# Kernel optimization log

Hardware: AMD Instinct MI355X
Metric: run time of the kernel (lower is better)

The kernel has to match this reference:

```python
import jax, jax.numpy as jnp
import numpy as np

B, K, HH, WW = 512, 256, 16, 16   # batch, channels (K//2 of init K=512), latent H, W
KH = 128                          # GRU hidden size
F = 16                            # future_window_lin


def gru_forward(seq, h0, W_ih, W_hh, b_ih, b_hh):
    # seq: (B,T,K) batch_first, h0: (B,KH). PyTorch GRU gate order: r, z, n.
    gx = jnp.einsum('btk,gk->btg', seq, W_ih) + b_ih  # (B,T,3*KH)

    def step(h, gx_t):
        gh = h @ W_hh.T + b_hh
        xr, xz, xn = jnp.split(gx_t, 3, axis=-1)
        hr, hz, hn = jnp.split(gh, 3, axis=-1)
        r = jax.nn.sigmoid(xr + hr)
        z = jax.nn.sigmoid(xz + hz)
        n = jnp.tanh(xn + r * hn)
        h_new = (1.0 - z) * n + z * h
        return h_new, h_new

    hT, outs = jax.lax.scan(step, h0, jnp.swapaxes(gx, 0, 1))  # outs: (T,B,KH)
    return jnp.swapaxes(outs, 0, 1), hT


def setup_inputs() -> dict:
    key = jax.random.key(0)
    ks = jax.random.split(key, 9)
    s = 0.05
    return {
        'z_q_x_st': jax.random.normal(ks[0], (B, K, HH, WW), jnp.float32),
        'z_e_x': jax.random.normal(ks[1], (B, K, HH, WW), jnp.float32),
        'z_q_x': jax.random.normal(ks[2], (B, K, HH, WW), jnp.float32),
        'hidden': jnp.zeros((1, B, KH), jnp.float32),
        'W_ih': jax.random.normal(ks[3], (3 * KH, K), jnp.float32) * s,
        'W_hh': jax.random.normal(ks[4], (3 * KH, KH), jnp.float32) * s,
        'b_ih': jnp.zeros((3 * KH,), jnp.float32),
        'b_hh': jnp.zeros((3 * KH,), jnp.float32),
        'Wk_w': jax.random.normal(ks[5], (F, K, KH), jnp.float32) * s,
        'Wk_b': jnp.zeros((F, K), jnp.float32),
        'p_sample': 100,
    }


def reference(z_q_x_st, z_e_x, z_q_x, hidden, W_ih, W_hh, b_ih, b_hh, Wk_w, Wk_b, p_sample):
    batch, k, h, w = z_e_x.shape
    f = Wk_w.shape[0]
    # (B,K,H,W) -> (B,H*W,K); row = idx//W, col = idx%W is just the row-major flat index
    z_flat = jnp.transpose(z_q_x_st, (0, 2, 3, 1)).reshape(batch, h * w, k)
    # encoded samples at flat positions p_sample+1 .. p_sample+F  -> (F,B,K)
    encoded = jnp.swapaxes(z_flat[:, p_sample + 1: p_sample + 1 + f, :], 0, 1)
    # GRU over the causal prefix; c_t = output at step p_sample (the last one)
    seq = z_flat[:, : p_sample + 1, :]
    out, _ = gru_forward(seq, hidden[0], W_ih, W_hh, b_ih, b_hh)
    c_t = out[:, -1, :]  # (B,KH)
    # per-step linear heads, batched: (F,B,K)
    pred = jnp.einsum('fkh,bh->fbk', Wk_w, c_t) + Wk_b[:, None, :]
    # totals[i] = encoded[i] @ pred[i].T  -> (F,B,B)
    totals = jnp.einsum('fbk,fck->fbc', encoded, pred)
    lsm = jax.nn.log_softmax(totals, axis=2)
    diag_sum = jnp.sum(jnp.diagonal(lsm, axis1=1, axis2=2))
    nce = -diag_sum / (batch * f)
    # 'correct' only reflects the last loop iteration in the torch code
    last = totals[-1]
    sm = jax.nn.softmax(last, axis=1)       # softmax over dim=1, then argmax over dim=0
    preds_idx = jnp.argmax(sm, axis=0)
    correct = jnp.sum(preds_idx == jnp.arange(batch))
    accuracy = correct.astype(jnp.float32) / batch
    return accuracy, nce, z_e_x, z_q_x
```

## Files before the change

kernel.cpp:

```cpp
#include <hip/hip_runtime.h>
#include <math.h>

#define NB_B   512
#define NK     256
#define NKH    128
#define NG3    384
#define NT     101
#define NF     16
#define NPASS  (512ull*256*256)

#define OFF_GX   0ull
#define N_GX     (512ull*101*384)
#define OFF_CT   (OFF_GX + N_GX)
#define OFF_ENC  (OFF_CT + 512ull*128)
#define OFF_PRED (OFF_ENC + 16ull*512*256)
#define OFF_TOT  (OFF_PRED + 16ull*512*256)
#define OFF_LSE  (OFF_TOT + 16ull*512*512)
#define OFF_DML  (OFF_LSE + 8192ull)
#define OFF_WT   (OFF_DML + 8192ull)
#define OFF_WKT  (OFF_WT + 384ull*256)
#define OFF_CNT  (OFF_WKT + 16ull*128*256)

__global__ __launch_bounds__(256) void k_transpose(
    const float* __restrict__ W_ih, const float* __restrict__ Wk_w,
    float* __restrict__ Wt, float* __restrict__ Wkt, int* __restrict__ cnt) {
  int idx = blockIdx.x * 256 + threadIdx.x;
  if (idx == 0) *cnt = 0;
  if (idx < 384 * 256) {
    int g = idx % 384, k = idx / 384;
    Wt[idx] = W_ih[g * 256 + k];
  }
  if (idx < 16 * 128 * 256) {
    int k = idx & 255, h = (idx >> 8) & 127, f = idx >> 15;
    Wkt[idx] = Wk_w[(f * 256 + k) * 128 + h];
  }
}

__global__ __launch_bounds__(768) void k_gx(
    const float* __restrict__ zq, const float* __restrict__ Wt,
    const float* __restrict__ b_ih, float* __restrict__ gx) {
  __shared__ float Xs[64][104];
  int b = blockIdx.x;
  int tid = threadIdx.x;
  int g = tid % 384;
  int th = tid / 384;
  int lane = tid & 63, wid = tid >> 6;
  float acc[52];
#pragma unroll
  for (int i = 0; i < 52; i++) acc[i] = 0.f;
  const float* zb = zq + (size_t)b * 65536;
  for (int kc = 0; kc < 4; kc++) {
    __syncthreads();
    for (int k = wid; k < 64; k += 12) {
      int kk = kc * 64 + k;
      Xs[k][lane] = zb[kk * 256 + lane];
      int t1 = 64 + lane;
      if (t1 < 104) Xs[k][t1] = (t1 < 101) ? zb[kk * 256 + t1] : 0.f;
    }
    __syncthreads();
    for (int k = 0; k < 64; k++) {
      float w = Wt[(kc * 64 + k) * 384 + g];
      const float4* xp = (const float4*)&Xs[k][th * 52];
#pragma unroll
      for (int i = 0; i < 13; i++) {
        float4 x = xp[i];
        acc[4 * i + 0] += w * x.x;
        acc[4 * i + 1] += w * x.y;
        acc[4 * i + 2] += w * x.z;
        acc[4 * i + 3] += w * x.w;
      }
    }
  }
  float bias = b_ih[g];
  int t0 = th * 52;
#pragma unroll
  for (int i = 0; i < 52; i++) {
    int t = t0 + i;
    if (t < 101) gx[(size_t)t * (512 * 384) + b * 384 + g] = acc[i] + bias;
  }
}

__global__ __launch_bounds__(768) void k_scan(
    const float* __restrict__ gx, const float* __restrict__ W_hh,
    const float* __restrict__ b_hh, const float* __restrict__ hidden,
    float* __restrict__ ct,
    const float* __restrict__ src0, const float* __restrict__ src1,
    float2* __restrict__ d0, float2* __restrict__ d1) {
  int tid = threadIdx.x;
  if (blockIdx.x >= 256) {
    const float4* S0 = (const float4*)src0;
    const float4* S1 = (const float4*)src1;
    const size_t n4 = NPASS / 4;
    const size_t stride = 256ull * 768;
    for (size_t i = (size_t)(blockIdx.x - 256) * 768 + tid; i < n4; i += stride) {
      float4 a = S0[i];
      float4 b = S1[i];
      d0[2 * i]     = make_float2(a.x, a.y);
      d0[2 * i + 1] = make_float2(a.z, a.w);
      d1[2 * i]     = make_float2(b.x, b.y);
      d1[2 * i + 1] = make_float2(b.z, b.w);
    }
    return;
  }
  __shared__ float hs[2][128];
  __shared__ float ghp[2][2][384];
  int b0 = blockIdx.x * 2;
  int g = tid % 384, kh = tid / 384;
  float4 w[16];
  const float4* wp = (const float4*)(W_hh + g * 128 + kh * 64);
#pragma unroll
  for (int i = 0; i < 16; i++) w[i] = wp[i];
  if (tid < 256) {
    int r = tid >> 7, k = tid & 127;
    hs[r][k] = hidden[(b0 + r) * 128 + k];
  }
  __syncthreads();
  for (int t = 0; t < 101; t++) {
    const float4* h0 = (const float4*)&hs[0][kh * 64];
    const float4* h1 = (const float4*)&hs[1][kh * 64];
    float a0 = 0.f, a1 = 0.f;
#pragma unroll
    for (int i = 0; i < 16; i++) {
      float4 wv = w[i], x0 = h0[i], x1 = h1[i];
      a0 += wv.x * x0.x + wv.y * x0.y + wv.z * x0.z + wv.w * x0.w;
      a1 += wv.x * x1.x + wv.y * x1.y + wv.z * x1.z + wv.w * x1.w;
    }
    ghp[0][kh][g] = a0;
    ghp[1][kh][g] = a1;
    __syncthreads();
    if (tid < 256) {
      int r = tid >> 7, k = tid & 127;
      const float* gxb = gx + (size_t)t * (512 * 384) + (b0 + r) * 384;
      float xr = gxb[k], xz = gxb[128 + k], xn = gxb[256 + k];
      float hr = ghp[r][0][k] + ghp[r][1][k] + b_hh[k];
      float hz = ghp[r][0][128 + k] + ghp[r][1][128 + k] + b_hh[128 + k];
      float hn = ghp[r][0][256 + k] + ghp[r][1][256 + k] + b_hh[256 + k];
      float rr = 1.f / (1.f + __expf(-(xr + hr)));
      float zz = 1.f / (1.f + __expf(-(xz + hz)));
      float nn = tanhf(xn + rr * hn);
      hs[r][k] = (1.f - zz) * nn + zz * hs[r][k];
    }
    __syncthreads();
  }
  if (tid < 256) {
    int r = tid >> 7, k = tid & 127;
    ct[(b0 + r) * 128 + k] = hs[r][k];
  }
}

__global__ __launch_bounds__(256) void k_enc(const float* __restrict__ zq,
                                             float* __restrict__ enc) {
  __shared__ float tile[256][17];
  int b = blockIdx.x, tid = threadIdx.x;
  const float* zb = zq + (size_t)b * 65536;
  for (int pass = 0; pass < 16; pass++) {
    int idx = pass * 256 + tid;
    int k = idx >> 4, f = idx & 15;
    tile[k][f] = zb[k * 256 + 101 + f];
  }
  __syncthreads();
  for (int f = 0; f < 16; f++)
    enc[(size_t)f * 131072 + b * 256 + tid] = tile[tid][f];
}

__global__ __launch_bounds__(256) void k_pred(
    const float* __restrict__ Wkt, const float* __restrict__ Wk_b,
    const float* __restrict__ ct, float* __restrict__ pred) {
  __shared__ float cts[32][128];
  int f = blockIdx.x, c0 = blockIdx.y * 32;
  int tid = threadIdx.x;
  for (int pass = 0; pass < 16; pass++) {
    int idx = pass * 256 + tid;
    int cc = idx >> 7, h = idx & 127;
    cts[cc][h] = ct[(c0 + cc) * 128 + h];
  }
  __syncthreads();
  float acc[32];
#pragma unroll
  for (int i = 0; i < 32; i++) acc[i] = 0.f;
  const float* wb = Wkt + (size_t)f * 32768 + tid;
  for (int h = 0; h < 128; h += 4) {
    float w0 = wb[(h + 0) * 256], w1 = wb[(h + 1) * 256];
    float w2 = wb[(h + 2) * 256], w3 = wb[(h + 3) * 256];
#pragma unroll
    for (int cc = 0; cc < 32; cc++) {
      float4 cv = *(const float4*)&cts[cc][h];
      acc[cc] += w0 * cv.x + w1 * cv.y + w2 * cv.z + w3 * cv.w;
    }
  }
  float bias = Wk_b[f * 256 + tid];
#pragma unroll
  for (int cc = 0; cc < 32; cc++)
    pred[((size_t)f * 512 + c0 + cc) * 256 + tid] = acc[cc] + bias;
}

__global__ __launch_bounds__(256) void k_totals(
    const float* __restrict__ enc, const float* __restrict__ pred,
    float* __restrict__ tot) {
  __shared__ float As[32][68];
  __shared__ float Bs[32][68];
  int f = blockIdx.z, b0 = blockIdx.y * 64, c0 = blockIdx.x * 64;
  int tid = threadIdx.x;
  int tx = tid & 15, ty = tid >> 4;
  float acc[4][4];
#pragma unroll
  for (int i = 0; i < 4; i++)
#pragma unroll
    for (int j = 0; j < 4; j++) acc[i][j] = 0.f;
  const float* Ab = enc + (size_t)f * 131072;
  const float* Bb = pred + (size_t)f * 131072;
  int lr = tid >> 3;
  int lc = (tid & 7) * 4;
  for (int kc = 0; kc < 8; kc++) {
    int k0 = kc * 32;
    __syncthreads();
    float4 av0 = *(const float4*)&Ab[(b0 + lr) * 256 + k0 + lc];
    float4 av1 = *(const float4*)&Ab[(b0 + 32 + lr) * 256 + k0 + lc];
    float4 bv0 = *(const float4*)&Bb[(c0 + lr) * 256 + k0 + lc];
    float4 bv1 = *(const float4*)&Bb[(c0 + 32 + lr) * 256 + k0 + lc];
    As[lc + 0][lr] = av0.x; As[lc + 1][lr] = av0.y;
    As[lc + 2][lr] = av0.z; As[lc + 3][lr] = av0.w;
    As[lc + 0][lr + 32] = av1.x; As[lc + 1][lr + 32] = av1.y;
    As[lc + 2][lr + 32] = av1.z; As[lc + 3][lr + 32] = av1.w;
    Bs[lc + 0][lr] = bv0.x; Bs[lc + 1][lr] = bv0.y;
    Bs[lc + 2][lr] = bv0.z; Bs[lc + 3][lr] = bv0.w;
    Bs[lc + 0][lr + 32] = bv1.x; Bs[lc + 1][lr + 32] = bv1.y;
    Bs[lc + 2][lr + 32] = bv1.z; Bs[lc + 3][lr + 32] = bv1.w;
    __syncthreads();
#pragma unroll
    for (int kk = 0; kk < 32; kk++) {
      float4 a = *(const float4*)&As[kk][ty * 4];
      float4 bq = *(const float4*)&Bs[kk][tx * 4];
      acc[0][0] += a.x * bq.x; acc[0][1] += a.x * bq.y;
      acc[0][2] += a.x * bq.z; acc[0][3] += a.x * bq.w;
      acc[1][0] += a.y * bq.x; acc[1][1] += a.y * bq.y;
      acc[1][2] += a.y * bq.z; acc[1][3] += a.y * bq.w;
      acc[2][0] += a.z * bq.x; acc[2][1] += a.z * bq.y;
      acc[2][2] += a.z * bq.z; acc[2][3] += a.z * bq.w;
      acc[3][0] += a.w * bq.x; acc[3][1] += a.w * bq.y;
      acc[3][2] += a.w * bq.z; acc[3][3] += a.w * bq.w;
    }
  }
#pragma unroll
  for (int i = 0; i < 4; i++) {
    float4 v = make_float4(acc[i][0], acc[i][1], acc[i][2], acc[i][3]);
    *(float4*)&tot[(size_t)f * 262144 + (b0 + ty * 4 + i) * 512 + c0 + tx * 4] = v;
  }
}

__global__ __launch_bounds__(64) void k_lse(const float* __restrict__ tot,
                                            float* __restrict__ lse,
                                            float* __restrict__ dml) {
  int row = blockIdx.x;
  int b = row & 511;
  int lane = threadIdx.x;
  const float* tr = tot + (size_t)row * 512;
  float v[8];
  float mx = -1e30f;
#pragma unroll
  for (int i = 0; i < 8; i++) { v[i] = tr[i * 64 + lane]; mx = fmaxf(mx, v[i]); }
#pragma unroll
  for (int s = 32; s > 0; s >>= 1) mx = fmaxf(mx, __shfl_xor(mx, s));
  float sum = 0.f;
#pragma unroll
  for (int i = 0; i < 8; i++) sum += __expf(v[i] - mx);
#pragma unroll
  for (int s = 32; s > 0; s >>= 1) sum += __shfl_xor(sum, s);
  if (lane == 0) {
    float l = __logf(sum) + mx;
    lse[row] = l;
    dml[row] = tr[b] - l;
  }
}

__global__ __launch_bounds__(64) void k_acc(const float* __restrict__ tot,
                                            const float* __restrict__ lse,
                                            int* __restrict__ cnt) {
  int c = blockIdx.x * 64 + threadIdx.x;
  const float* t15 = tot + (size_t)15 * 262144;
  const float* l15 = lse + 15 * 512;
  float best = -1e30f;
  int bi = 0;
  for (int b = 0; b < 512; b++) {
    float v = t15[(size_t)b * 512 + c] - l15[b];
    if (v > best) { best = v; bi = b; }
  }
  if (bi == c) atomicAdd(cnt, 1);
}

__global__ __launch_bounds__(256) void k_fin(const float* __restrict__ dml,
                                             const int* __restrict__ cnt,
                                             float* __restrict__ out) {
  __shared__ float red[256];
  int tid = threadIdx.x;
  float s = 0.f;
  for (int i = tid; i < 8192; i += 256) s += dml[i];
  red[tid] = s;
  __syncthreads();
  for (int st = 128; st > 0; st >>= 1) {
    if (tid < st) red[tid] += red[tid + st];
    __syncthreads();
  }
  if (tid == 0) {
    out[1] = -red[0] / 8192.f;
    out[0] = (float)(*cnt) / 512.f;
  }
}

extern "C" void kernel_launch(void* const* d_in, const int* in_sizes, int n_in,
                              void* d_out, int out_size, void* d_ws, size_t ws_size,
                              hipStream_t stream) {
  const float* zq   = (const float*)d_in[0];
  const float* ze   = (const float*)d_in[1];
  const float* zqx  = (const float*)d_in[2];
  const float* hid  = (const float*)d_in[3];
  const float* W_ih = (const float*)d_in[4];
  const float* W_hh = (const float*)d_in[5];
  const float* b_ih = (const float*)d_in[6];
  const float* b_hh = (const float*)d_in[7];
  const float* Wk_w = (const float*)d_in[8];
  const float* Wk_b = (const float*)d_in[9];
  float* out = (float*)d_out;
  float* ws  = (float*)d_ws;

  k_transpose<<<2048, 256, 0, stream>>>(W_ih, Wk_w, ws + OFF_WT, ws + OFF_WKT,
                                        (int*)(ws + OFF_CNT));
  k_gx<<<512, 768, 0, stream>>>(zq, ws + OFF_WT, b_ih, ws + OFF_GX);
  k_scan<<<512, 768, 0, stream>>>(ws + OFF_GX, W_hh, b_hh, hid, ws + OFF_CT,
                                  ze, zqx,
                                  (float2*)(out + 2), (float2*)(out + 2 + NPASS));
  k_enc<<<512, 256, 0, stream>>>(zq, ws + OFF_ENC);
  k_pred<<<dim3(16, 16), 256, 0, stream>>>(ws + OFF_WKT, Wk_b, ws + OFF_CT, ws + OFF_PRED);
  k_totals<<<dim3(8, 8, 16), 256, 0, stream>>>(ws + OFF_ENC, ws + OFF_PRED, ws + OFF_TOT);
  k_lse<<<8192, 64, 0, stream>>>(ws + OFF_TOT, ws + OFF_LSE, ws + OFF_DML);
  k_acc<<<8, 64, 0, stream>>>(ws + OFF_TOT, ws + OFF_LSE, (int*)(ws + OFF_CNT));
  k_fin<<<1, 256, 0, stream>>>(ws + OFF_DML, (const int*)(ws + OFF_CNT), out);
}
```

Baseline: 981.7 us.

## Retile gx GEMM with shared-memory weights, split copy loop, parallelize argmax

The input-projection kernel now stages 32-row weight tiles in shared memory, and each thread computes a 4-gate by 13-timestep register tile with float4 stores. This replaces the per-thread scalar global weight load of the old layout. The passthrough copy in the scan kernel now moves float2 chunks from two halves of the buffer instead of float4 loads split into float2 stores. The accuracy kernel changes from 8 blocks of serial 512-long loops to one wave per column with a shuffle argmax reduction and first-index tie-break, which raises parallelism in a tiny tail kernel.

```diff
diff --git a/kernel.cpp b/kernel.cpp
--- a/kernel.cpp
+++ b/kernel.cpp
@@ -39,44 +39,57 @@
 __global__ __launch_bounds__(768) void k_gx(
     const float* __restrict__ zq, const float* __restrict__ Wt,
     const float* __restrict__ b_ih, float* __restrict__ gx) {
-  __shared__ float Xs[64][104];
+  __shared__ float Xs[32][104];
+  __shared__ float Ws[32 * 384];
   int b = blockIdx.x;
   int tid = threadIdx.x;
-  int g = tid % 384;
-  int th = tid / 384;
+  int q = tid % 96;
+  int tt = tid / 96;
+  int g0 = q * 4;
+  int t0 = tt * 13;
   int lane = tid & 63, wid = tid >> 6;
-  float acc[52];
-#pragma unroll
-  for (int i = 0; i < 52; i++) acc[i] = 0.f;
+  float acc[4][13];
+#pragma unroll
+  for (int i = 0; i < 4; i++)
+#pragma unroll
+    for (int j = 0; j < 13; j++) acc[i][j] = 0.f;
   const float* zb = zq + (size_t)b * 65536;
-  for (int kc = 0; kc < 4; kc++) {
-    __syncthreads();
-    for (int k = wid; k < 64; k += 12) {
-      int kk = kc * 64 + k;
+  for (int kc = 0; kc < 8; kc++) {
+    __syncthreads();
+    for (int k = wid; k < 32; k += 12) {
+      int kk = kc * 32 + k;
       Xs[k][lane] = zb[kk * 256 + lane];
       int t1 = 64 + lane;
       if (t1 < 104) Xs[k][t1] = (t1 < 101) ? zb[kk * 256 + t1] : 0.f;
     }
-    __syncthreads();
-    for (int k = 0; k < 64; k++) {
-      float w = Wt[(kc * 64 + k) * 384 + g];
-      const float4* xp = (const float4*)&Xs[k][th * 52];
-#pragma unroll
-      for (int i = 0; i < 13; i++) {
-        float4 x = xp[i];
-        acc[4 * i + 0] += w * x.x;
-        acc[4 * i + 1] += w * x.y;
-        acc[4 * i + 2] += w * x.z;
-        acc[4 * i + 3] += w * x.w;
+    {
+      const float4* wsrc = (const float4*)(Wt + (size_t)kc * 32 * 384);
+      float4* wdst = (float4*)Ws;
+      for (int i = tid; i < 3072; i += 768) wdst[i] = wsrc[i];
+    }
+    __syncthreads();
+    for (int k = 0; k < 32; k++) {
+      float4 w = *(const float4*)&Ws[k * 384 + g0];
+      const float* xr = &Xs[k][t0];
+#pragma unroll
+      for (int j = 0; j < 13; j++) {
+        float x = xr[j];
+        acc[0][j] += w.x * x;
+        acc[1][j] += w.y * x;
+        acc[2][j] += w.z * x;
+        acc[3][j] += w.w * x;
       }
     }
   }
-  float bias = b_ih[g];
-  int t0 = th * 52;
-#pragma unroll
-  for (int i = 0; i < 52; i++) {
-    int t = t0 + i;
-    if (t < 101) gx[(size_t)t * (512 * 384) + b * 384 + g] = acc[i] + bias;
+  float4 bias = *(const float4*)&b_ih[g0];
+#pragma unroll
+  for (int j = 0; j < 13; j++) {
+    int t = t0 + j;
+    if (t < 101) {
+      float4 v = make_float4(acc[0][j] + bias.x, acc[1][j] + bias.y,
+                             acc[2][j] + bias.z, acc[3][j] + bias.w);
+      *(float4*)&gx[(size_t)t * (512 * 384) + b * 384 + g0] = v;
+    }
   }
 }
 
@@ -88,17 +101,19 @@
     float2* __restrict__ d0, float2* __restrict__ d1) {
   int tid = threadIdx.x;
   if (blockIdx.x >= 256) {
-    const float4* S0 = (const float4*)src0;
-    const float4* S1 = (const float4*)src1;
-    const size_t n4 = NPASS / 4;
+    const float2* S0 = (const float2*)src0;
+    const float2* S1 = (const float2*)src1;
+    const size_t half = NPASS / 4;
     const size_t stride = 256ull * 768;
-    for (size_t i = (size_t)(blockIdx.x - 256) * 768 + tid; i < n4; i += stride) {
-      float4 a = S0[i];
-      float4 b = S1[i];
-      d0[2 * i]     = make_float2(a.x, a.y);
-      d0[2 * i + 1] = make_float2(a.z, a.w);
-      d1[2 * i]     = make_float2(b.x, b.y);
-      d1[2 * i + 1] = make_float2(b.z, b.w);
+    for (size_t i = (size_t)(blockIdx.x - 256) * 768 + tid; i < half; i += stride) {
+      float2 a = S0[i];
+      float2 b2 = S0[i + half];
+      float2 c = S1[i];
+      float2 d = S1[i + half];
+      d0[i] = a;
+      d0[i + half] = b2;
+      d1[i] = c;
+      d1[i + half] = d;
     }
     return;
   }
@@ -276,16 +291,22 @@
 __global__ __launch_bounds__(64) void k_acc(const float* __restrict__ tot,
                                             const float* __restrict__ lse,
                                             int* __restrict__ cnt) {
-  int c = blockIdx.x * 64 + threadIdx.x;
+  int c = blockIdx.x;
+  int lane = threadIdx.x;
   const float* t15 = tot + (size_t)15 * 262144;
   const float* l15 = lse + 15 * 512;
   float best = -1e30f;
-  int bi = 0;
-  for (int b = 0; b < 512; b++) {
+  int bi = 1 << 30;
+  for (int b = lane; b < 512; b += 64) {
     float v = t15[(size_t)b * 512 + c] - l15[b];
     if (v > best) { best = v; bi = b; }
   }
-  if (bi == c) atomicAdd(cnt, 1);
+  for (int s = 32; s > 0; s >>= 1) {
+    float ov = __shfl_xor(best, s);
+    int oi = __shfl_xor(bi, s);
+    if (ov > best || (ov == best && oi < bi)) { best = ov; bi = oi; }
+  }
+  if (lane == 0 && bi == c) atomicAdd(cnt, 1);
 }
 
 __global__ __launch_bounds__(256) void k_fin(const float* __restrict__ dml,
@@ -333,6 +354,6 @@
   k_pred<<<dim3(16, 16), 256, 0, stream>>>(ws + OFF_WKT, Wk_b, ws + OFF_CT, ws + OFF_PRED);
   k_totals<<<dim3(8, 8, 16), 256, 0, stream>>>(ws + OFF_ENC, ws + OFF_PRED, ws + OFF_TOT);
   k_lse<<<8192, 64, 0, stream>>>(ws + OFF_TOT, ws + OFF_LSE, ws + OFF_DML);
-  k_acc<<<8, 64, 0, stream>>>(ws + OFF_TOT, ws + OFF_LSE, (int*)(ws + OFF_CNT));
+  k_acc<<<512, 64, 0, stream>>>(ws + OFF_TOT, ws + OFF_LSE, (int*)(ws + OFF_CNT));
   k_fin<<<1, 256, 0, stream>>>(ws + OFF_DML, (const int*)(ws + OFF_CNT), out);
 }
```

After: 913.5 us. 1.07x faster.
